# Performance work log

Hardware: AMD Instinct MI355X
Metric: run time of the kernel (lower is better)

## Reference

```python
import jax, jax.numpy as jnp
import numpy as np

MARGIN_M = 0.5   # ArcFace additive angular margin
SCALE_S = 64.0   # ArcFace logit scale


def _l2norm(x, axis=-1, eps=1e-12):
    return x / jnp.sqrt(jnp.sum(x * x, axis=axis, keepdims=True) + eps)


def _arcface_ce(logits, labels):
    """Apply ArcFace margin at target column, scale, softmax-CE. logits [B,C], labels [B]."""
    B = logits.shape[0]
    rows = jnp.arange(B)
    t = logits[rows, labels]                          # target cosine, [B]
    tc = jnp.clip(t, -1.0 + 1e-7, 1.0 - 1e-7)
    cos_m, sin_m = np.cos(MARGIN_M), np.sin(MARGIN_M)
    # cos(theta + m); hard-margin fallback: t - sin(pi-m)*m when t <= cos(pi-m)
    marg = tc * cos_m - jnp.sqrt(1.0 - tc * tc) * sin_m
    thresh = np.cos(np.pi - MARGIN_M)
    mm = np.sin(np.pi - MARGIN_M) * MARGIN_M
    final_t = jnp.where(t > thresh, marg, t - mm)
    logits_m = logits.at[rows, labels].set(final_t) * SCALE_S   # [B, C]
    logp = jax.nn.log_softmax(logits_m, axis=1)
    return -jnp.mean(logp[rows, labels])


def setup_inputs() -> dict:
    key = jax.random.key(0)
    k1, k2, k3 = jax.random.split(key, 3)
    B, D, C, RD = 256, 512, 100000, 8
    return {
        "local_embeddings": jax.random.normal(k1, (B, D), dtype=jnp.float32),
        "weight": jax.random.normal(k2, (C, D), dtype=jnp.float32) * 0.01,
        "local_labels": jax.random.randint(k3, (B, RD), 0, C, dtype=jnp.int64),
        "random_diff": RD,
    }


def reference(local_embeddings, weight, local_labels, random_diff):
    B = local_embeddings.shape[0]
    # no_grad label-column shuffle: keep 3 random columns out of random_diff
    noise = jax.random.uniform(jax.random.key(42), (B, random_diff))
    ids_keep = jnp.argsort(noise, axis=1)[:, :3]                       # [B, 3]
    labels3 = jnp.take_along_axis(local_labels, ids_keep, axis=1)      # [B, 3]
    # world_size=1, sample_rate=1: all labels are positive local indices
    norm_emb = _l2norm(local_embeddings)                               # [B, D]
    norm_w = _l2norm(weight)                                           # [C, D]
    logits = jnp.clip(norm_emb @ norm_w.T, -1.0, 1.0)                  # [B, C]
    loss = (_arcface_ce(logits, labels3[:, 0])
            + _arcface_ce(logits, labels3[:, 1])
            + _arcface_ce(logits, labels3[:, 2])) / 3.0
    return loss
```

## Files before the change

### kernel.cpp

```cpp
#include <hip/hip_runtime.h>
#include <hip/hip_bf16.h>
#include <stdint.h>

#define K_D 512
#define N_C 100000
#define SCALE 64.0f

#define COS_M 0.87758256189037271612f
#define SIN_M 0.47942553860420300027f
#define TH   (-0.87758256189037271612f)
#define MM_C  0.23971276930210150013f

typedef __attribute__((ext_vector_type(8))) short bf16x8;
typedef __attribute__((ext_vector_type(4))) float f32x4;

#define NB 1563
#define ZSTRIDE 1568

#define OFF_INVNE 0
#define OFF_EMB   1024
#define OFF_TP    263168
#define OFF_ZROW  269312
#define OFF_ZPART 270336

__device__ __forceinline__ uint32_t f2bf(float f) {
    __hip_bfloat16 h = __float2bfloat16(f);
    return (uint32_t)__builtin_bit_cast(ushort, h);
}

__global__ __launch_bounds__(256) void prep_emb(const float* __restrict__ E,
                                                ushort* __restrict__ Ebf,
                                                float* __restrict__ invne) {
    int w = threadIdx.x >> 6, lane = threadIdx.x & 63;
    int row = blockIdx.x * 4 + w;
    const float4* src = (const float4*)(E + (size_t)row * K_D);
    float4 a = src[2 * lane];
    float4 b = src[2 * lane + 1];
    float ss = a.x*a.x + a.y*a.y + a.z*a.z + a.w*a.w
             + b.x*b.x + b.y*b.y + b.z*b.z + b.w*b.w;
    #pragma unroll
    for (int m = 32; m >= 1; m >>= 1) ss += __shfl_xor(ss, m, 64);
    uint4 pk;
    pk.x = f2bf(a.x) | (f2bf(a.y) << 16);
    pk.y = f2bf(a.z) | (f2bf(a.w) << 16);
    pk.z = f2bf(b.x) | (f2bf(b.y) << 16);
    pk.w = f2bf(b.z) | (f2bf(b.w) << 16);
    const int kstep = lane >> 2, gg = lane & 3;
    const size_t slot = ((size_t)(row >> 4) * 16 + kstep) * 64 + (row & 15) + (gg << 4);
    ((uint4*)Ebf)[slot] = pk;
    if (lane == 0) invne[row] = rsqrtf(ss + 1e-12f);
}

__device__ __forceinline__ void threefry(uint32_t x0, uint32_t x1, uint32_t& o0, uint32_t& o1) {
    const uint32_t k0 = 0u, k1 = 42u;
    const uint32_t k2 = k0 ^ k1 ^ 0x1BD11BDAu;
    const uint32_t ks[3] = {k0, k1, k2};
    x0 += k0; x1 += k1;
    const int rot0[4] = {13, 15, 26, 6};
    const int rot1[4] = {17, 29, 16, 24};
    #pragma unroll
    for (int grp = 0; grp < 5; ++grp) {
        const int* r = (grp & 1) ? rot1 : rot0;
        #pragma unroll
        for (int i = 0; i < 4; ++i) {
            x0 += x1;
            x1 = (x1 << r[i]) | (x1 >> (32 - r[i]));
            x1 ^= x0;
        }
        x0 += ks[(grp + 1) % 3];
        x1 += ks[(grp + 2) % 3] + (uint32_t)(grp + 1);
    }
    o0 = x0; o1 = x1;
}

__global__ __launch_bounds__(256) void target_kernel(const float* __restrict__ E,
                                                     const float* __restrict__ W,
                                                     const int* __restrict__ ll,
                                                     float* __restrict__ tp) {
    int w = threadIdx.x >> 6, lane = threadIdx.x & 63;
    int p = blockIdx.x * 4 + w;
    int b = p / 3;
    int jj = p - b * 3;
    float u[8];
    #pragma unroll
    for (int j = 0; j < 8; ++j) {
        int n = b * 8 + j;
        uint32_t x0, x1, o0, o1;
        if (n < 1024) { x0 = (uint32_t)n; x1 = (uint32_t)(n + 1024); }
        else          { x0 = (uint32_t)(n - 1024); x1 = (uint32_t)n; }
        threefry(x0, x1, o0, o1);
        uint32_t bits = (n < 1024) ? o0 : o1;
        uint32_t fb = (bits >> 9) | 0x3F800000u;
        u[j] = __builtin_bit_cast(float, fb) - 1.0f;
    }
    bool used[8] = {false,false,false,false,false,false,false,false};
    int sel = 0;
    for (int s = 0; s <= jj; ++s) {
        float bv = 2.0f; int bi = 0;
        for (int i = 0; i < 8; ++i)
            if (!used[i] && u[i] < bv) { bv = u[i]; bi = i; }
        used[bi] = true;
        sel = bi;
    }
    int c = ll[b * 8 + sel];

    const float4* ep = (const float4*)(E + (size_t)b * K_D);
    const float4* wp = (const float4*)(W + (size_t)c * K_D);
    float4 e0 = ep[lane], e1 = ep[lane + 64];
    float4 w0 = wp[lane], w1 = wp[lane + 64];
    float dot = e0.x*w0.x + e0.y*w0.y + e0.z*w0.z + e0.w*w0.w
              + e1.x*w1.x + e1.y*w1.y + e1.z*w1.z + e1.w*w1.w;
    float esq = e0.x*e0.x + e0.y*e0.y + e0.z*e0.z + e0.w*e0.w
              + e1.x*e1.x + e1.y*e1.y + e1.z*e1.z + e1.w*e1.w;
    float wsq = w0.x*w0.x + w0.y*w0.y + w0.z*w0.z + w0.w*w0.w
              + w1.x*w1.x + w1.y*w1.y + w1.z*w1.z + w1.w*w1.w;
    #pragma unroll
    for (int m = 32; m >= 1; m >>= 1) {
        dot += __shfl_xor(dot, m, 64);
        esq += __shfl_xor(esq, m, 64);
        wsq += __shfl_xor(wsq, m, 64);
    }
    if (lane == 0) {
        float t = dot * rsqrtf(esq + 1e-12f) * rsqrtf(wsq + 1e-12f);
        t = fminf(1.0f, fmaxf(-1.0f, t));
        float tc = fminf(1.0f - 1e-7f, fmaxf(-1.0f + 1e-7f, t));
        float marg = tc * COS_M - sqrtf(fmaxf(0.0f, 1.0f - tc * tc)) * SIN_M;
        float ft = (t > TH) ? marg : (t - MM_C);
        tp[p * 2]     = t;
        tp[p * 2 + 1] = ft;
    }
}

__global__ __launch_bounds__(256, 2) void gemm_z(const float* __restrict__ W,
                                                 const ushort* __restrict__ Ebf,
                                                 const float* __restrict__ invne,
                                                 float* __restrict__ zpart) {
    __shared__ ushort Wt[2][32 * 512];
    __shared__ float ine_lds[256];
    __shared__ float sp[2][2][32];
    __shared__ float inw_lds[2][32];

    const int tid  = threadIdx.x;
    const int lane = tid & 63, wv = tid >> 6;
    const int r16  = lane & 15, g = lane >> 4;
    const int nb   = blockIdx.x;
    const int cb   = nb * 64;

    ine_lds[tid] = invne[tid];

    const int cg = wv & 1, kh = wv >> 1;

    #define BARRIER() { asm volatile("s_waitcnt lgkmcnt(0)" ::: "memory"); \
                        __builtin_amdgcn_s_barrier(); }

    #define ISSUE(PF, CH)                                                       \
        {                                                                       \
            const int cls = cb + (CH) * 32 + cg * 16 + r16;                     \
            const float* wsrc = W + (size_t)(cls < N_C ? cls : N_C - 1) * K_D   \
                                  + g * 8;                                      \
            _Pragma("unroll")                                                   \
            for (int t = 0; t < 8; ++t) {                                       \
                PF[2*t]   = *(const float4*)(wsrc + (2*t + kh) * 32);           \
                PF[2*t+1] = *(const float4*)(wsrc + (2*t + kh) * 32 + 4);       \
            }                                                                   \
        }

    #define PROCESS(PF, B)                                                      \
        {                                                                       \
            float ssq = 0.f;                                                    \
            _Pragma("unroll")                                                   \
            for (int t = 0; t < 8; ++t) {                                       \
                float4 A = PF[2*t], Bv = PF[2*t+1];                             \
                ssq += A.x*A.x + A.y*A.y + A.z*A.z + A.w*A.w                    \
                     + Bv.x*Bv.x + Bv.y*Bv.y + Bv.z*Bv.z + Bv.w*Bv.w;           \
                uint4 pk;                                                       \
                pk.x = f2bf(A.x)  | (f2bf(A.y)  << 16);                         \
                pk.y = f2bf(A.z)  | (f2bf(A.w)  << 16);                         \
                pk.z = f2bf(Bv.x) | (f2bf(Bv.y) << 16);                         \
                pk.w = f2bf(Bv.z) | (f2bf(Bv.w) << 16);                         \
                *(uint4*)&Wt[B][(cg * 16 + 2*t + kh) * 512 + lane * 8] = pk;    \
            }                                                                   \
            ssq += __shfl_xor(ssq, 16, 64);                                     \
            ssq += __shfl_xor(ssq, 32, 64);                                     \
            if (g == 0) sp[B][kh][cg * 16 + r16] = ssq;                         \
        }

    float zacc[4][4] = {};

    #define COMPUTE(B, CH)                                                      \
        {                                                                       \
            const ushort* ab = Ebf + (size_t)wv * 32768 + (size_t)lane * 8;     \
            const ushort* bb = &Wt[B][lane * 8];                                \
            f32x4 acc[4][2] = {};                                               \
            _Pragma("unroll 4")                                                 \
            for (int ks = 0; ks < 16; ++ks) {                                   \
                bf16x8 b0 = *(const bf16x8*)(bb + ks * 512);                    \
                bf16x8 b1 = *(const bf16x8*)(bb + (16 + ks) * 512);             \
                _Pragma("unroll")                                               \
                for (int m = 0; m < 4; ++m) {                                   \
                    bf16x8 a = *(const bf16x8*)(ab + m * 8192 + ks * 512);      \
                    acc[m][0] = __builtin_amdgcn_mfma_f32_16x16x32_bf16(        \
                                    a, b0, acc[m][0], 0, 0, 0);                 \
                    acc[m][1] = __builtin_amdgcn_mfma_f32_16x16x32_bf16(        \
                                    a, b1, acc[m][1], 0, 0, 0);                 \
                }                                                               \
            }                                                                   \
            const float iw0 = inw_lds[B][r16];                                  \
            const float iw1 = inw_lds[B][16 + r16];                             \
            const bool v0 = (cb + (CH) * 32 + r16) < N_C;                       \
            const bool v1 = (cb + (CH) * 32 + 16 + r16) < N_C;                  \
            _Pragma("unroll")                                                   \
            for (int m = 0; m < 4; ++m) {                                       \
                _Pragma("unroll")                                               \
                for (int i = 0; i < 4; ++i) {                                   \
                    const float ine = ine_lds[wv * 64 + m * 16 + g * 4 + i];    \
                    float c0 = acc[m][0][i] * iw0 * ine;                        \
                    float c1 = acc[m][1][i] * iw1 * ine;                        \
                    c0 = fminf(1.0f, fmaxf(-1.0f, c0));                         \
                    c1 = fminf(1.0f, fmaxf(-1.0f, c1));                         \
                    float e0 = v0 ? __expf(SCALE * c0 - 64.0f) : 0.f;           \
                    float e1 = v1 ? __expf(SCALE * c1 - 64.0f) : 0.f;           \
                    zacc[m][i] += e0 + e1;                                      \
                }                                                               \
            }                                                                   \
        }

    float4 pfa[16], pfb[16];

    ISSUE(pfa, 0);
    PROCESS(pfa, 0);
    BARRIER();
    if (tid < 32) inw_lds[0][tid] = rsqrtf(sp[0][0][tid] + sp[0][1][tid] + 1e-12f);
    ISSUE(pfb, 1);
    BARRIER();
    COMPUTE(0, 0);
    PROCESS(pfb, 1);
    BARRIER();
    if (tid < 32) inw_lds[1][tid] = rsqrtf(sp[1][0][tid] + sp[1][1][tid] + 1e-12f);
    BARRIER();
    COMPUTE(1, 1);

    #undef ISSUE
    #undef PROCESS
    #undef COMPUTE
    #undef BARRIER

    #pragma unroll
    for (int m = 0; m < 4; ++m)
        #pragma unroll
        for (int i = 0; i < 4; ++i) {
            float v = zacc[m][i];
            v += __shfl_xor(v, 1, 64);
            v += __shfl_xor(v, 2, 64);
            v += __shfl_xor(v, 4, 64);
            v += __shfl_xor(v, 8, 64);
            if (r16 == m * 4 + i) {
                const int row = wv * 64 + m * 16 + g * 4 + i;
                zpart[(size_t)row * ZSTRIDE + nb] = v;
            }
        }
}

__global__ __launch_bounds__(256) void zrow_kernel(const float* __restrict__ zpart,
                                                   float* __restrict__ zrow) {
    const int b = blockIdx.x;
    float sum = 0.f;
    for (int t = threadIdx.x; t < NB; t += 256)
        sum += zpart[(size_t)b * ZSTRIDE + t];
    __shared__ float red[256];
    red[threadIdx.x] = sum;
    __syncthreads();
    for (int st = 128; st >= 1; st >>= 1) {
        if (threadIdx.x < st) red[threadIdx.x] += red[threadIdx.x + st];
        __syncthreads();
    }
    if (threadIdx.x == 0) zrow[b] = red[0];
}

__global__ __launch_bounds__(256) void loss_kernel(const float* __restrict__ zrow,
                                                   const float* __restrict__ tp,
                                                   float* __restrict__ out) {
    const int b = threadIdx.x;
    const float Z = zrow[b];
    float lsum = 0.f;
    #pragma unroll
    for (int j = 0; j < 3; ++j) {
        float t  = tp[(b * 3 + j) * 2];
        float ft = tp[(b * 3 + j) * 2 + 1];
        float S = Z - expf(SCALE * t - 64.0f) + expf(SCALE * ft - 64.0f);
        lsum += logf(S) + 64.0f - SCALE * ft;
    }
    __shared__ float red[256];
    red[b] = lsum;
    __syncthreads();
    for (int st = 128; st >= 1; st >>= 1) {
        if (b < st) red[b] += red[b + st];
        __syncthreads();
    }
    if (b == 0) out[0] = red[0] / 768.0f;
}

extern "C" void kernel_launch(void* const* d_in, const int* in_sizes, int n_in,
                              void* d_out, int out_size, void* d_ws, size_t ws_size,
                              hipStream_t stream) {
    const float* E = (const float*)d_in[0];
    const float* W = (const float*)d_in[1];
    const int*  LL = (const int*)d_in[2];
    char* ws = (char*)d_ws;
    float*  invne = (float*)(ws + OFF_INVNE);
    ushort* Ebf   = (ushort*)(ws + OFF_EMB);
    float*  tp    = (float*)(ws + OFF_TP);
    float*  zrow  = (float*)(ws + OFF_ZROW);
    float*  zpart = (float*)(ws + OFF_ZPART);
    float*  out   = (float*)d_out;

    hipLaunchKernelGGL(prep_emb,      dim3(64),   dim3(256), 0, stream, E, Ebf, invne);
    hipLaunchKernelGGL(target_kernel, dim3(192),  dim3(256), 0, stream, E, W, LL, tp);
    hipLaunchKernelGGL(gemm_z,        dim3(NB),   dim3(256), 0, stream, W, Ebf, invne, zpart);
    hipLaunchKernelGGL(zrow_kernel,   dim3(256),  dim3(256), 0, stream, zpart, zrow);
    hipLaunchKernelGGL(loss_kernel,   dim3(1),    dim3(256), 0, stream, zrow, tp, out);
}
```

Before: 111.6 us.

## Keep embedding tiles in registers and pipeline four class chunks per 512-thread block

The GEMM kernel now uses 512-thread blocks covering 128 classes each in four 32-class chunks. Each wave holds its 32 embedding rows as bf16 fragments in registers for the whole block instead of reloading them from global memory per chunk. The W loads are spread across waves with coalesced row reads, double-buffered through LDS, and overlapped with the MFMA/exp work of the previous chunk. The cost is heavy register use (32 bf16x8 A fragments plus prefetch buffers), which may limit occupancy or cause spills, and the partial-sum width is halved.

```diff
diff --git a/kernel.cpp b/kernel.cpp
--- a/kernel.cpp
+++ b/kernel.cpp
@@ -14,8 +14,8 @@
 typedef __attribute__((ext_vector_type(8))) short bf16x8;
 typedef __attribute__((ext_vector_type(4))) float f32x4;
 
-#define NB 1563
-#define ZSTRIDE 1568
+#define NNB 782
+#define ZSTRIDE 784
 
 #define OFF_INVNE 0
 #define OFF_EMB   1024
@@ -131,131 +131,142 @@
     }
 }
 
-__global__ __launch_bounds__(256, 2) void gemm_z(const float* __restrict__ W,
+__global__ __launch_bounds__(512, 2) void gemm_z(const float* __restrict__ W,
                                                  const ushort* __restrict__ Ebf,
                                                  const float* __restrict__ invne,
                                                  float* __restrict__ zpart) {
     __shared__ ushort Wt[2][32 * 512];
-    __shared__ float ine_lds[256];
-    __shared__ float sp[2][2][32];
-    __shared__ float inw_lds[2][32];
+    __shared__ float sp[2][32];
 
     const int tid  = threadIdx.x;
     const int lane = tid & 63, wv = tid >> 6;
     const int r16  = lane & 15, g = lane >> 4;
     const int nb   = blockIdx.x;
-    const int cb   = nb * 64;
-
-    ine_lds[tid] = invne[tid];
-
-    const int cg = wv & 1, kh = wv >> 1;
-
-    #define BARRIER() { asm volatile("s_waitcnt lgkmcnt(0)" ::: "memory"); \
-                        __builtin_amdgcn_s_barrier(); }
-
-    #define ISSUE(PF, CH)                                                       \
+    const int cb   = nb * 128;
+
+    float4 pf[4][2];
+
+    #define ISSUE(CH)                                                           \
+        if ((CH) < 4) {                                                         \
+            _Pragma("unroll")                                                   \
+            for (int rr = 0; rr < 4; ++rr) {                                    \
+                int cls = cb + (CH) * 32 + wv * 4 + rr;                         \
+                const float4* src = (const float4*)(W +                         \
+                    (size_t)(cls < N_C ? cls : N_C - 1) * K_D);                 \
+                pf[rr][0] = src[lane];                                          \
+                pf[rr][1] = src[lane + 64];                                     \
+            }                                                                   \
+        }
+
+    ISSUE(0);
+
+    bf16x8 areg[2][16];
+    #pragma unroll
+    for (int mt = 0; mt < 2; ++mt)
+        #pragma unroll
+        for (int ks = 0; ks < 16; ++ks)
+            areg[mt][ks] = *(const bf16x8*)(Ebf
+                + (size_t)(wv * 2 + mt) * 8192 + ks * 512 + lane * 8);
+
+    float inew[2][4];
+    #pragma unroll
+    for (int mt = 0; mt < 2; ++mt)
+        #pragma unroll
+        for (int i = 0; i < 4; ++i)
+            inew[mt][i] = invne[wv * 32 + mt * 16 + g * 4 + i];
+
+    float zacc[2][4] = {};
+
+    #define PROCESS(CH)                                                         \
         {                                                                       \
-            const int cls = cb + (CH) * 32 + cg * 16 + r16;                     \
-            const float* wsrc = W + (size_t)(cls < N_C ? cls : N_C - 1) * K_D   \
-                                  + g * 8;                                      \
+            const int B = (CH) & 1;                                             \
             _Pragma("unroll")                                                   \
-            for (int t = 0; t < 8; ++t) {                                       \
-                PF[2*t]   = *(const float4*)(wsrc + (2*t + kh) * 32);           \
-                PF[2*t+1] = *(const float4*)(wsrc + (2*t + kh) * 32 + 4);       \
+            for (int rr = 0; rr < 4; ++rr) {                                    \
+                const int cl32 = wv * 4 + rr;                                   \
+                const int nt = cl32 >> 4, cl = cl32 & 15;                       \
+                float4 a4 = pf[rr][0], b4 = pf[rr][1];                          \
+                float s = a4.x*a4.x + a4.y*a4.y + a4.z*a4.z + a4.w*a4.w         \
+                        + b4.x*b4.x + b4.y*b4.y + b4.z*b4.z + b4.w*b4.w;        \
+                _Pragma("unroll")                                               \
+                for (int m = 32; m >= 1; m >>= 1) s += __shfl_xor(s, m, 64);    \
+                if (lane == 0) sp[B][cl32] = s;                                 \
+                _Pragma("unroll")                                               \
+                for (int h = 0; h < 2; ++h) {                                   \
+                    const int k4 = h * 64 + lane;                               \
+                    const int ks = k4 >> 3, gg = (k4 >> 1) & 3, hf = k4 & 1;    \
+                    float4 v = pf[rr][h];                                       \
+                    uint2 pk;                                                   \
+                    pk.x = f2bf(v.x) | (f2bf(v.y) << 16);                       \
+                    pk.y = f2bf(v.z) | (f2bf(v.w) << 16);                       \
+                    *(uint2*)&Wt[B][(nt * 16 + ks) * 512 + (cl + gg * 16) * 8   \
+                                    + hf * 4] = pk;                             \
+                }                                                               \
             }                                                                   \
         }
 
-    #define PROCESS(PF, B)                                                      \
+    #define COMPUTE(CH)                                                         \
         {                                                                       \
-            float ssq = 0.f;                                                    \
+            const int B = (CH) & 1;                                             \
+            f32x4 acc00 = {}, acc01 = {}, acc10 = {}, acc11 = {};               \
+            const ushort* bb = &Wt[B][lane * 8];                                \
             _Pragma("unroll")                                                   \
-            for (int t = 0; t < 8; ++t) {                                       \
-                float4 A = PF[2*t], Bv = PF[2*t+1];                             \
-                ssq += A.x*A.x + A.y*A.y + A.z*A.z + A.w*A.w                    \
-                     + Bv.x*Bv.x + Bv.y*Bv.y + Bv.z*Bv.z + Bv.w*Bv.w;           \
-                uint4 pk;                                                       \
-                pk.x = f2bf(A.x)  | (f2bf(A.y)  << 16);                         \
-                pk.y = f2bf(A.z)  | (f2bf(A.w)  << 16);                         \
-                pk.z = f2bf(Bv.x) | (f2bf(Bv.y) << 16);                         \
-                pk.w = f2bf(Bv.z) | (f2bf(Bv.w) << 16);                         \
-                *(uint4*)&Wt[B][(cg * 16 + 2*t + kh) * 512 + lane * 8] = pk;    \
-            }                                                                   \
-            ssq += __shfl_xor(ssq, 16, 64);                                     \
-            ssq += __shfl_xor(ssq, 32, 64);                                     \
-            if (g == 0) sp[B][kh][cg * 16 + r16] = ssq;                         \
-        }
-
-    float zacc[4][4] = {};
-
-    #define COMPUTE(B, CH)                                                      \
-        {                                                                       \
-            const ushort* ab = Ebf + (size_t)wv * 32768 + (size_t)lane * 8;     \
-            const ushort* bb = &Wt[B][lane * 8];                                \
-            f32x4 acc[4][2] = {};                                               \
-            _Pragma("unroll 4")                                                 \
             for (int ks = 0; ks < 16; ++ks) {                                   \
                 bf16x8 b0 = *(const bf16x8*)(bb + ks * 512);                    \
-                bf16x8 b1 = *(const bf16x8*)(bb + (16 + ks) * 512);             \
+                bf16x8 b1 = *(const bf16x8*)(bb + 8192 + ks * 512);             \
+                acc00 = __builtin_amdgcn_mfma_f32_16x16x32_bf16(                \
+                            areg[0][ks], b0, acc00, 0, 0, 0);                   \
+                acc01 = __builtin_amdgcn_mfma_f32_16x16x32_bf16(                \
+                            areg[1][ks], b0, acc01, 0, 0, 0);                   \
+                acc10 = __builtin_amdgcn_mfma_f32_16x16x32_bf16(                \
+                            areg[0][ks], b1, acc10, 0, 0, 0);                   \
+                acc11 = __builtin_amdgcn_mfma_f32_16x16x32_bf16(                \
+                            areg[1][ks], b1, acc11, 0, 0, 0);                   \
+            }                                                                   \
+            _Pragma("unroll")                                                   \
+            for (int nt = 0; nt < 2; ++nt) {                                    \
+                const int cls = cb + (CH) * 32 + nt * 16 + r16;                 \
+                const float iw = rsqrtf(sp[B][nt * 16 + r16] + 1e-12f);         \
+                const bool vld = cls < N_C;                                     \
                 _Pragma("unroll")                                               \
-                for (int m = 0; m < 4; ++m) {                                   \
-                    bf16x8 a = *(const bf16x8*)(ab + m * 8192 + ks * 512);      \
-                    acc[m][0] = __builtin_amdgcn_mfma_f32_16x16x32_bf16(        \
-                                    a, b0, acc[m][0], 0, 0, 0);                 \
-                    acc[m][1] = __builtin_amdgcn_mfma_f32_16x16x32_bf16(        \
-                                    a, b1, acc[m][1], 0, 0, 0);                 \
+                for (int i = 0; i < 4; ++i) {                                   \
+                    float c0 = (nt ? acc10[i] : acc00[i]) * iw * inew[0][i];    \
+                    float c1 = (nt ? acc11[i] : acc01[i]) * iw * inew[1][i];    \
+                    c0 = fminf(1.0f, fmaxf(-1.0f, c0));                         \
+                    c1 = fminf(1.0f, fmaxf(-1.0f, c1));                         \
+                    zacc[0][i] += vld ? __expf(SCALE * c0 - 64.0f) : 0.f;       \
+                    zacc[1][i] += vld ? __expf(SCALE * c1 - 64.0f) : 0.f;       \
                 }                                                               \
             }                                                                   \
-            const float iw0 = inw_lds[B][r16];                                  \
-            const float iw1 = inw_lds[B][16 + r16];                             \
-            const bool v0 = (cb + (CH) * 32 + r16) < N_C;                       \
-            const bool v1 = (cb + (CH) * 32 + 16 + r16) < N_C;                  \
-            _Pragma("unroll")                                                   \
-            for (int m = 0; m < 4; ++m) {                                       \
-                _Pragma("unroll")                                               \
-                for (int i = 0; i < 4; ++i) {                                   \
-                    const float ine = ine_lds[wv * 64 + m * 16 + g * 4 + i];    \
-                    float c0 = acc[m][0][i] * iw0 * ine;                        \
-                    float c1 = acc[m][1][i] * iw1 * ine;                        \
-                    c0 = fminf(1.0f, fmaxf(-1.0f, c0));                         \
-                    c1 = fminf(1.0f, fmaxf(-1.0f, c1));                         \
-                    float e0 = v0 ? __expf(SCALE * c0 - 64.0f) : 0.f;           \
-                    float e1 = v1 ? __expf(SCALE * c1 - 64.0f) : 0.f;           \
-                    zacc[m][i] += e0 + e1;                                      \
-                }                                                               \
-            }                                                                   \
-        }
-
-    float4 pfa[16], pfb[16];
-
-    ISSUE(pfa, 0);
-    PROCESS(pfa, 0);
-    BARRIER();
-    if (tid < 32) inw_lds[0][tid] = rsqrtf(sp[0][0][tid] + sp[0][1][tid] + 1e-12f);
-    ISSUE(pfb, 1);
-    BARRIER();
-    COMPUTE(0, 0);
-    PROCESS(pfb, 1);
-    BARRIER();
-    if (tid < 32) inw_lds[1][tid] = rsqrtf(sp[1][0][tid] + sp[1][1][tid] + 1e-12f);
-    BARRIER();
-    COMPUTE(1, 1);
+        }
+
+    #define PHASE_END() { asm volatile("s_waitcnt lgkmcnt(0)" ::: "memory");    \
+                          __builtin_amdgcn_s_barrier();                         \
+                          __builtin_amdgcn_sched_barrier(0); }
+
+    PROCESS(0);
+    ISSUE(1);
+    PHASE_END();
+    COMPUTE(0);  PROCESS(1);  ISSUE(2);  PHASE_END();
+    COMPUTE(1);  PROCESS(2);  ISSUE(3);  PHASE_END();
+    COMPUTE(2);  PROCESS(3);             PHASE_END();
+    COMPUTE(3);
 
     #undef ISSUE
     #undef PROCESS
     #undef COMPUTE
-    #undef BARRIER
-
-    #pragma unroll
-    for (int m = 0; m < 4; ++m)
+    #undef PHASE_END
+
+    #pragma unroll
+    for (int mt = 0; mt < 2; ++mt)
         #pragma unroll
         for (int i = 0; i < 4; ++i) {
-            float v = zacc[m][i];
+            float v = zacc[mt][i];
             v += __shfl_xor(v, 1, 64);
             v += __shfl_xor(v, 2, 64);
             v += __shfl_xor(v, 4, 64);
             v += __shfl_xor(v, 8, 64);
-            if (r16 == m * 4 + i) {
-                const int row = wv * 64 + m * 16 + g * 4 + i;
+            if (r16 == mt * 4 + i) {
+                const int row = wv * 32 + mt * 16 + g * 4 + i;
                 zpart[(size_t)row * ZSTRIDE + nb] = v;
             }
         }
@@ -265,7 +276,7 @@
                                                    float* __restrict__ zrow) {
     const int b = blockIdx.x;
     float sum = 0.f;
-    for (int t = threadIdx.x; t < NB; t += 256)
+    for (int t = threadIdx.x; t < NNB; t += 256)
         sum += zpart[(size_t)b * ZSTRIDE + t];
     __shared__ float red[256];
     red[threadIdx.x] = sum;
@@ -316,7 +327,7 @@
 
     hipLaunchKernelGGL(prep_emb,      dim3(64),   dim3(256), 0, stream, E, Ebf, invne);
     hipLaunchKernelGGL(target_kernel, dim3(192),  dim3(256), 0, stream, E, W, LL, tp);
-    hipLaunchKernelGGL(gemm_z,        dim3(NB),   dim3(256), 0, stream, W, Ebf, invne, zpart);
+    hipLaunchKernelGGL(gemm_z,        dim3(NNB),  dim3(512), 0, stream, W, Ebf, invne, zpart);
     hipLaunchKernelGGL(zrow_kernel,   dim3(256),  dim3(256), 0, stream, zpart, zrow);
     hipLaunchKernelGGL(loss_kernel,   dim3(1),    dim3(256), 0, stream, zrow, tp, out);
 }
```

New measurement: 97.73 us. 12.4% less time.
